# Kernel tuning notes

Measured on AMD Instinct MI355X. Metric: run time of the kernel, lower is better.

The kernel has to match this reference:

```python
import jax, jax.numpy as jnp
import numpy as np

H_IMG, W_IMG = 2160, 3840


def _avgpool3x3(x):
    # AvgPool2d(3, stride=1, padding=1), count_include_pad=True -> divide by 9 always
    s = jax.lax.reduce_window(x, 0.0, jax.lax.add, (3, 3, 1), (1, 1, 1), 'SAME')
    return s / 9.0


def setup_inputs() -> dict:
    key = jax.random.key(0)
    k1, k2, k3, k4 = jax.random.split(key, 4)
    depth = jax.random.uniform(k1, (H_IMG, W_IMG), jnp.float32) * 4.0 + 0.5
    rgb = jax.random.uniform(k2, (H_IMG, W_IMG, 3), jnp.float32)
    mask = jax.random.randint(k3, (H_IMG, W_IMG), 0, 2, jnp.int32)
    l = jax.random.normal(k4, (9, 3), jnp.float32) * 0.3
    fx = fy = 3000.0
    cx, cy = W_IMG / 2.0, H_IMG / 2.0
    CameraParam = jnp.array([[fx, 0.0, cx], [0.0, fy, cy], [0.0, 0.0, 1.0]], jnp.float32)
    return {'depth': depth, 'rgb': rgb, 'mask': mask, 'l': l, 'CameraParam': CameraParam}


def reference(depth, rgb, mask, l, CameraParam):
    nrows, ncols = depth.shape
    imask = mask > 0                      # [H, W] bool
    m3 = imask[..., None]                 # [H, W, 1]

    # Homogeneous pixel grid -> back-projected rays (precomputed in torch __init__)
    yy, xx = jnp.meshgrid(jnp.arange(nrows, dtype=jnp.float32),
                          jnp.arange(ncols, dtype=jnp.float32), indexing='ij')
    p2d = jnp.stack([xx, yy, jnp.ones_like(xx)], axis=-1)      # [H, W, 3]
    Kinv = jnp.linalg.inv(CameraParam)
    p3d = jnp.einsum('ij,hwj->hwi', Kinv, p2d)                 # [H, W, 3]

    # Depth -> 3D points, shifted neighbors (zero-padded at borders)
    p = p3d * depth[..., None]                                 # [H, W, 3]
    pl = jnp.pad(p[:, 1:, :], ((0, 0), (0, 1), (0, 0)))        # right neighbor
    pu = jnp.pad(p[1:, :, :], ((0, 1), (0, 0), (0, 0)))        # down neighbor

    n = jnp.cross(pl - p, pu - p)                              # [H, W, 3]
    norm = jnp.linalg.norm(n, axis=-1, keepdims=True)
    n = n / jnp.maximum(norm, 1e-12)                           # F.normalize

    nx, ny, nz = n[..., 0], n[..., 1], n[..., 2]
    ones = jnp.ones_like(nx)
    Hsh = jnp.stack([ones, ny, nz, nx, nx * ny, ny * nz,
                     -nx * nx - ny * ny + 2.0 * nz * nz,
                     nz * nx, nx * nx - ny * ny], axis=-1)     # [H, W, 9]
    B = jnp.einsum('hwk,kc->hwc', Hsh, l)                      # [H, W, 3]

    # Scatter into full image: zero outside mask (matches render_img[imask] = B)
    render = jnp.where(m3, B, 0.0)
    render_mean = jax.lax.stop_gradient(_avgpool3x3(render))   # render_img.detach()
    rgbmean = _avgpool3x3(jax.lax.stop_gradient(rgb))          # rgb.detach()

    diff = (render - render_mean) - (rgb - rgbmean)
    cnt = jnp.sum(imask).astype(jnp.float32) * 3.0             # MSE over masked elems
    loss = jnp.sum(jnp.where(m3, diff * diff, 0.0)) / cnt
    return loss
```

## Files before the change

### kernel.cpp

```cpp
#include <hip/hip_runtime.h>
#include <math.h>

#define H_IMG 2160
#define W_IMG 3840
#define SPAN 252
#define NSX 16
#define HS 12
#define WPB 4
#define NSY 45
#define NBLOCKS (NSX * NSY)
#define NBINS 2048

__global__ __launch_bounds__(256, 3) void shading_main(
    const float* __restrict__ depth,
    const float* __restrict__ rgb,
    const int*   __restrict__ mask,
    const float* __restrict__ lmat,
    const float* __restrict__ K,
    float* __restrict__ accum,
    int direct)
{
    const int tid  = threadIdx.x;
    const int lane = tid & 63;
    const int wv   = tid >> 6;
    const int sx   = blockIdx.x;
    const int x0   = sx * SPAN;
    const int y0   = blockIdx.y * (WPB * HS) + wv * HS;
    const int colBase = x0 + 4 * lane;
    const bool fullIn = (colBase + 3) < W_IMG;

    const float m00 = K[0], m01 = K[1], m02 = K[2];
    const float m10 = K[3], m11 = K[4], m12 = K[5];
    const float m20 = K[6], m21 = K[7], m22 = K[8];
    const float det = m00*(m11*m22 - m12*m21)
                    - m01*(m10*m22 - m12*m20)
                    + m02*(m10*m21 - m11*m20);
    const float id  = 1.0f / det;
    const float i00 = (m11*m22 - m12*m21) * id;
    const float i01 = (m02*m21 - m01*m22) * id;
    const float i02 = (m01*m12 - m02*m11) * id;
    const float i10 = (m12*m20 - m10*m22) * id;
    const float i11 = (m00*m22 - m02*m20) * id;
    const float i12 = (m02*m10 - m00*m12) * id;
    const float i20 = (m10*m21 - m11*m20) * id;
    const float i21 = (m01*m20 - m00*m21) * id;
    const float i22 = (m00*m11 - m01*m10) * id;

    float L[27];
    #pragma unroll
    for (int i = 0; i < 27; ++i) L[i] = lmat[i];

    float wout[4];
    #pragma unroll
    for (int k = 0; k < 4; ++k) {
        const int c  = colBase + k;
        const int lc = 4 * lane + k;
        const bool v = (c < W_IMG) && (lc <= SPAN) && (lc >= 1 || sx == 0);
        wout[k] = v ? 1.0f : 0.0f;
    }
    const float qm1s = (lane == 0) ? 0.0f : 1.0f;

    float rx = fmaf(i00, (float)colBase, fmaf(i01, (float)(y0 - 1), i02));
    float ry = fmaf(i10, (float)colBase, fmaf(i11, (float)(y0 - 1), i12));
    float rz = fmaf(i20, (float)colBase, fmaf(i21, (float)(y0 - 1), i22));

    const float4 Z4 = make_float4(0.f, 0.f, 0.f, 0.f);

    float4 dC = Z4, dN = Z4;
    float4 raC = Z4, rbC = Z4, rcC = Z4;
    int4   mC  = make_int4(0, 0, 0, 0);
    if (fullIn) {
        if (y0 > 0) {
            const long pix = (long)(y0 - 1) * W_IMG + colBase;
            dC  = *(const float4*)(depth + pix);
            raC = *(const float4*)(rgb + pix * 3);
            rbC = *(const float4*)(rgb + pix * 3 + 4);
            rcC = *(const float4*)(rgb + pix * 3 + 8);
            mC  = *(const int4*)(mask + pix);
        }
        dN = *(const float4*)(depth + (long)y0 * W_IMG + colBase);
    }

    float sA0[4] = {0,0,0,0}, sA1[4] = {0,0,0,0}, sA2[4] = {0,0,0,0};
    float sB0[4] = {0,0,0,0}, sB1[4] = {0,0,0,0}, sB2[4] = {0,0,0,0};
    float qB0[4] = {0,0,0,0}, qB1[4] = {0,0,0,0}, qB2[4] = {0,0,0,0};
    float wB[4]  = {0,0,0,0};
    float accS = 0.f, accC = 0.f;

    #pragma unroll 1
    for (int j = 0; j < HS + 2; ++j) {
        const int h = y0 - 1 + j;

        float4 dP = Z4, raN = Z4, rbN = Z4, rcN = Z4;
        int4   mN = make_int4(0, 0, 0, 0);
        if (fullIn) {
            if (h + 2 < H_IMG)
                dP = *(const float4*)(depth + (long)(h + 2) * W_IMG + colBase);
            if (h + 1 < H_IMG) {
                const long pix = (long)(h + 1) * W_IMG + colBase;
                raN = *(const float4*)(rgb + pix * 3);
                rbN = *(const float4*)(rgb + pix * 3 + 4);
                rcN = *(const float4*)(rgb + pix * 3 + 8);
                mN  = *(const int4*)(mask + pix);
            }
        }

        const float dcv[4] = {dC.x, dC.y, dC.z, dC.w};
        const float dnv[4] = {dN.x, dN.y, dN.z, dN.w};
        const float rrv[12] = {raC.x, raC.y, raC.z, raC.w,
                               rbC.x, rbC.y, rbC.z, rbC.w,
                               rcC.x, rcC.y, rcC.z, rcC.w};
        const int   mmv[4] = {mC.x, mC.y, mC.z, mC.w};
        const float dcR = __shfl_down(dC.x, 1, 64);

        float qC0[4], qC1[4], qC2[4], wC[4];
        float rxk = rx, ryk = ry, rzk = rz;
        #pragma unroll
        for (int k = 0; k < 4; ++k) {
            const float d0 = dcv[k];
            const float dR = (k < 3) ? dcv[k + 1] : dcR;
            const float dD = dnv[k];
            const float px = rxk * d0, py = ryk * d0, pz = rzk * d0;
            const float ax = (rxk + i00) * dR - px;
            const float ay = (ryk + i10) * dR - py;
            const float az = (rzk + i20) * dR - pz;
            const float bx = (rxk + i01) * dD - px;
            const float by = (ryk + i11) * dD - py;
            const float bz = (rzk + i21) * dD - pz;
            float nx = ay*bz - az*by;
            float ny = az*bx - ax*bz;
            float nz = ax*by - ay*bx;
            const float nn  = nx*nx + ny*ny + nz*nz;
            const float inr = __builtin_amdgcn_rsqf(fmaxf(nn, 1e-24f));
            nx *= inr; ny *= inr; nz *= inr;
            const float h4 = nx*ny, h5 = ny*nz, h7 = nz*nx;
            const float nx2 = nx*nx, ny2 = ny*ny, nz2 = nz*nz;
            const float h6 = 2.f*nz2 - nx2 - ny2;
            const float h8 = nx2 - ny2;
            const float B0 = L[0] + ny*L[3] + nz*L[6] + nx*L[9]  + h4*L[12] + h5*L[15] + h6*L[18] + h7*L[21] + h8*L[24];
            const float B1 = L[1] + ny*L[4] + nz*L[7] + nx*L[10] + h4*L[13] + h5*L[16] + h6*L[19] + h7*L[22] + h8*L[25];
            const float B2 = L[2] + ny*L[5] + nz*L[8] + nx*L[11] + h4*L[14] + h5*L[17] + h6*L[20] + h7*L[23] + h8*L[26];
            const float m  = (mmv[k] > 0) ? 1.0f : 0.0f;
            qC0[k] = fmaf(m, B0, -rrv[3*k + 0]);
            qC1[k] = fmaf(m, B1, -rrv[3*k + 1]);
            qC2[k] = fmaf(m, B2, -rrv[3*k + 2]);
            wC[k]  = m * wout[k];
            rxk += i00; ryk += i10; rzk += i20;
        }

        float sC0[4], sC1[4], sC2[4];
        {
            const float a0 = __shfl_up(qC0[3], 1, 64) * qm1s;
            const float a1 = __shfl_up(qC1[3], 1, 64) * qm1s;
            const float a2 = __shfl_up(qC2[3], 1, 64) * qm1s;
            const float p0 = __shfl_down(qC0[0], 1, 64);
            const float p1 = __shfl_down(qC1[0], 1, 64);
            const float p2 = __shfl_down(qC2[0], 1, 64);

            const float t01_0 = qC0[0] + qC0[1];
            const float t12_0 = qC0[1] + qC0[2];
            const float t23_0 = qC0[2] + qC0[3];
            sC0[0] = a0 + t01_0;
            sC0[1] = t01_0 + qC0[2];
            sC0[2] = t12_0 + qC0[3];
            sC0[3] = t23_0 + p0;

            const float t01_1 = qC1[0] + qC1[1];
            const float t12_1 = qC1[1] + qC1[2];
            const float t23_1 = qC1[2] + qC1[3];
            sC1[0] = a1 + t01_1;
            sC1[1] = t01_1 + qC1[2];
            sC1[2] = t12_1 + qC1[3];
            sC1[3] = t23_1 + p1;

            const float t01_2 = qC2[0] + qC2[1];
            const float t12_2 = qC2[1] + qC2[2];
            const float t23_2 = qC2[2] + qC2[3];
            sC2[0] = a2 + t01_2;
            sC2[1] = t01_2 + qC2[2];
            sC2[2] = t12_2 + qC2[3];
            sC2[3] = t23_2 + p2;
        }

        if (j >= 2) {
            #pragma unroll
            for (int k = 0; k < 4; ++k) {
                const float v0 = sA0[k] + sB0[k] + sC0[k];
                const float v1 = sA1[k] + sB1[k] + sC1[k];
                const float v2 = sA2[k] + sB2[k] + sC2[k];
                const float d0 = fmaf(v0, -(1.f/9.f), qB0[k]);
                const float d1 = fmaf(v1, -(1.f/9.f), qB1[k]);
                const float d2 = fmaf(v2, -(1.f/9.f), qB2[k]);
                const float w  = wB[k];
                accS = fmaf(w, d0*d0 + d1*d1 + d2*d2, accS);
                accC += w;
            }
        }

        #pragma unroll
        for (int k = 0; k < 4; ++k) {
            sA0[k] = sB0[k]; sA1[k] = sB1[k]; sA2[k] = sB2[k];
            sB0[k] = sC0[k]; sB1[k] = sC1[k]; sB2[k] = sC2[k];
            qB0[k] = qC0[k]; qB1[k] = qC1[k]; qB2[k] = qC2[k];
            wB[k]  = wC[k];
        }
        dC = dN; dN = dP;
        raC = raN; rbC = rbN; rcC = rcN; mC = mN;
        rx += i01; ry += i11; rz += i21;
    }

    #pragma unroll
    for (int off = 32; off > 0; off >>= 1) {
        accS += __shfl_down(accS, off, 64);
        accC += __shfl_down(accC, off, 64);
    }
    __shared__ float sS[WPB], sC[WPB];
    if (lane == 0) { sS[wv] = accS; sC[wv] = accC; }
    __syncthreads();
    if (tid == 0) {
        const float ts = sS[0] + sS[1] + sS[2] + sS[3];
        const float tc = sC[0] + sC[1] + sC[2] + sC[3];
        const int bid = blockIdx.y * gridDim.x + blockIdx.x;
        if (direct) {
            accum[2*bid + 0] = ts;
            accum[2*bid + 1] = tc;
        } else {
            const int bin = bid & (NBINS - 1);
            atomicAdd(&accum[2*bin + 0], ts);
            atomicAdd(&accum[2*bin + 1], tc);
        }
    }
}

__global__ __launch_bounds__(256) void finalize_kernel(
    const float* __restrict__ part, int n, float* __restrict__ out)
{
    const int tid = threadIdx.x;
    float s = 0.f, c = 0.f;
    for (int i = tid; i < n; i += 256) {
        s += part[2*i + 0];
        c += part[2*i + 1];
    }
    #pragma unroll
    for (int off = 32; off > 0; off >>= 1) {
        s += __shfl_down(s, off, 64);
        c += __shfl_down(c, off, 64);
    }
    __shared__ float sS[4], sC[4];
    const int wid = tid >> 6, lane = tid & 63;
    if (lane == 0) { sS[wid] = s; sC[wid] = c; }
    __syncthreads();
    if (tid == 0) {
        const float ts = sS[0] + sS[1] + sS[2] + sS[3];
        const float tc = sC[0] + sC[1] + sC[2] + sC[3];
        out[0] = ts / (3.0f * tc);
    }
}

extern "C" void kernel_launch(void* const* d_in, const int* in_sizes, int n_in,
                              void* d_out, int out_size, void* d_ws, size_t ws_size,
                              hipStream_t stream) {
    const float* depth = (const float*)d_in[0];
    const float* rgb   = (const float*)d_in[1];
    const int*   mask  = (const int*)  d_in[2];
    const float* lmat  = (const float*)d_in[3];
    const float* K     = (const float*)d_in[4];
    float* accum = (float*)d_ws;
    float* out   = (float*)d_out;

    const dim3 grid(NSX, NSY);

    if (ws_size >= (size_t)NBLOCKS * 2 * sizeof(float)) {
        shading_main<<<grid, 256, 0, stream>>>(depth, rgb, mask, lmat, K, accum, 1);
        finalize_kernel<<<1, 256, 0, stream>>>(accum, NBLOCKS, out);
    } else {
        hipMemsetAsync(accum, 0, NBINS * 2 * sizeof(float), stream);
        shading_main<<<grid, 256, 0, stream>>>(depth, rgb, mask, lmat, K, accum, 0);
        finalize_kernel<<<1, 256, 0, stream>>>(accum, NBINS, out);
    }
}
```

Baseline: 209.0 us.

## Unroll row loop by two with ping-pong registers and relax launch bounds

The row-streaming loop is restructured into pairs of rows, with even and odd register sets that swap roles through a macro body. This removes the per-iteration register rotation of the 3-row window (partial sums, centre values, weights, depth, rgb and mask). Next-row loads are now issued after the normal computation instead of at the top of the loop. Launch bounds drop from 3 to 2 blocks per CU, giving more registers per thread at the cost of occupancy and latency hiding.

Result: no change. 207.3 us (-0.8%).

```diff
diff --git a/kernel.cpp b/kernel.cpp
--- a/kernel.cpp
+++ b/kernel.cpp
@@ -9,9 +9,10 @@
 #define WPB 4
 #define NSY 45
 #define NBLOCKS (NSX * NSY)
+#define NPAIR ((HS + 2) / 2)
 #define NBINS 2048
 
-__global__ __launch_bounds__(256, 3) void shading_main(
+__global__ __launch_bounds__(256, 2) void shading_main(
     const float* __restrict__ depth,
     const float* __restrict__ rgb,
     const int*   __restrict__ mask,
@@ -26,7 +27,8 @@
     const int sx   = blockIdx.x;
     const int x0   = sx * SPAN;
     const int y0   = blockIdx.y * (WPB * HS) + wv * HS;
-    const int colBase = x0 + 4 * lane;
+    const int colBase  = x0 + 4 * lane;
+    const int colBase3 = 3 * colBase;
     const bool fullIn = (colBase + 3) < W_IMG;
 
     const float m00 = K[0], m01 = K[1], m02 = K[2];
@@ -66,148 +68,164 @@
 
     const float4 Z4 = make_float4(0.f, 0.f, 0.f, 0.f);
 
-    float4 dC = Z4, dN = Z4;
-    float4 raC = Z4, rbC = Z4, rcC = Z4;
-    int4   mC  = make_int4(0, 0, 0, 0);
+    float4 dP = Z4, dQ = Z4;
+    float4 raE = Z4, rbE = Z4, rcE = Z4;  int4 mE = make_int4(0,0,0,0);
+    float4 raO = Z4, rbO = Z4, rcO = Z4;  int4 mO = make_int4(0,0,0,0);
+
     if (fullIn) {
-        if (y0 > 0) {
-            const long pix = (long)(y0 - 1) * W_IMG + colBase;
-            dC  = *(const float4*)(depth + pix);
-            raC = *(const float4*)(rgb + pix * 3);
-            rbC = *(const float4*)(rgb + pix * 3 + 4);
-            rcC = *(const float4*)(rgb + pix * 3 + 8);
-            mC  = *(const int4*)(mask + pix);
+        if (y0 > 0 && (y0 - 1) < H_IMG) {
+            const float* dr = depth + (size_t)(y0 - 1) * W_IMG;
+            const float* rr = rgb   + (size_t)(y0 - 1) * (3 * W_IMG);
+            const int*   mr = mask  + (size_t)(y0 - 1) * W_IMG;
+            dP  = *(const float4*)(dr + colBase);
+            raE = *(const float4*)(rr + colBase3);
+            rbE = *(const float4*)(rr + colBase3 + 4);
+            rcE = *(const float4*)(rr + colBase3 + 8);
+            mE  = *(const int4*)(mr + colBase);
         }
-        dN = *(const float4*)(depth + (long)y0 * W_IMG + colBase);
-    }
-
-    float sA0[4] = {0,0,0,0}, sA1[4] = {0,0,0,0}, sA2[4] = {0,0,0,0};
-    float sB0[4] = {0,0,0,0}, sB1[4] = {0,0,0,0}, sB2[4] = {0,0,0,0};
-    float qB0[4] = {0,0,0,0}, qB1[4] = {0,0,0,0}, qB2[4] = {0,0,0,0};
-    float wB[4]  = {0,0,0,0};
+        if (y0 < H_IMG) {
+            const float* dr = depth + (size_t)y0 * W_IMG;
+            const float* rr = rgb   + (size_t)y0 * (3 * W_IMG);
+            const int*   mr = mask  + (size_t)y0 * W_IMG;
+            dQ  = *(const float4*)(dr + colBase);
+            raO = *(const float4*)(rr + colBase3);
+            rbO = *(const float4*)(rr + colBase3 + 4);
+            rcO = *(const float4*)(rr + colBase3 + 8);
+            mO  = *(const int4*)(mr + colBase);
+        }
+    }
+
+    float sE0[4]={0,0,0,0}, sE1[4]={0,0,0,0}, sE2[4]={0,0,0,0};
+    float sO0[4]={0,0,0,0}, sO1[4]={0,0,0,0}, sO2[4]={0,0,0,0};
+    float qE0[4]={0,0,0,0}, qE1[4]={0,0,0,0}, qE2[4]={0,0,0,0};
+    float qO0[4]={0,0,0,0}, qO1[4]={0,0,0,0}, qO2[4]={0,0,0,0};
+    float wE[4]={0,0,0,0},  wO[4]={0,0,0,0};
     float accS = 0.f, accC = 0.f;
 
+#define BODY(DCUR, DNXT, RA, RB, RC, MM, QM0,QM1,QM2, QO0_,QO1_,QO2_, WM, WO_, \
+             SM0,SM1,SM2, SO0_,SO1_,SO2_, ISSROW, DO_EMIT) do {                \
+    const float dcv[4] = {DCUR.x, DCUR.y, DCUR.z, DCUR.w};                     \
+    const float dnv[4] = {DNXT.x, DNXT.y, DNXT.z, DNXT.w};                     \
+    const float rrv[12] = {RA.x,RA.y,RA.z,RA.w, RB.x,RB.y,RB.z,RB.w,           \
+                           RC.x,RC.y,RC.z,RC.w};                               \
+    const int   mmv[4] = {MM.x, MM.y, MM.z, MM.w};                             \
+    const float dcR = __shfl_down(DCUR.x, 1, 64);                              \
+    float rxk = rx, ryk = ry, rzk = rz;                                        \
+    _Pragma("unroll")                                                          \
+    for (int k = 0; k < 4; ++k) {                                              \
+        const float d0 = dcv[k];                                               \
+        const float dR = (k < 3) ? dcv[k + 1] : dcR;                           \
+        const float dD = dnv[k];                                               \
+        const float px = rxk * d0, py = ryk * d0, pz = rzk * d0;               \
+        const float ax = (rxk + i00) * dR - px;                                \
+        const float ay = (ryk + i10) * dR - py;                                \
+        const float az = (rzk + i20) * dR - pz;                                \
+        const float bx = (rxk + i01) * dD - px;                                \
+        const float by = (ryk + i11) * dD - py;                                \
+        const float bz = (rzk + i21) * dD - pz;                                \
+        float nx = ay*bz - az*by;                                              \
+        float ny = az*bx - ax*bz;                                              \
+        float nz = ax*by - ay*bx;                                              \
+        const float nn  = nx*nx + ny*ny + nz*nz;                               \
+        const float inr = __builtin_amdgcn_rsqf(fmaxf(nn, 1e-24f));            \
+        nx *= inr; ny *= inr; nz *= inr;                                       \
+        const float h4 = nx*ny, h5 = ny*nz, h7 = nz*nx;                        \
+        const float nx2 = nx*nx, ny2 = ny*ny, nz2 = nz*nz;                     \
+        const float h6 = 2.f*nz2 - nx2 - ny2;                                  \
+        const float h8 = nx2 - ny2;                                            \
+        const float B0 = L[0] + ny*L[3] + nz*L[6] + nx*L[9]  + h4*L[12]        \
+                       + h5*L[15] + h6*L[18] + h7*L[21] + h8*L[24];            \
+        const float B1 = L[1] + ny*L[4] + nz*L[7] + nx*L[10] + h4*L[13]        \
+                       + h5*L[16] + h6*L[19] + h7*L[22] + h8*L[25];            \
+        const float B2 = L[2] + ny*L[5] + nz*L[8] + nx*L[11] + h4*L[14]        \
+                       + h5*L[17] + h6*L[20] + h7*L[23] + h8*L[26];            \
+        const float m  = (mmv[k] > 0) ? 1.0f : 0.0f;                           \
+        QM0[k] = fmaf(m, B0, -rrv[3*k + 0]);                                   \
+        QM1[k] = fmaf(m, B1, -rrv[3*k + 1]);                                   \
+        QM2[k] = fmaf(m, B2, -rrv[3*k + 2]);                                   \
+        WM[k]  = m * wout[k];                                                  \
+        rxk += i00; ryk += i10; rzk += i20;                                    \
+    }                                                                          \
+             \
+    {                                                                          \
+        const int hI = (ISSROW);                                               \
+        DCUR = Z4; RA = Z4; RB = Z4; RC = Z4; MM = make_int4(0,0,0,0);         \
+        if (fullIn && hI < H_IMG) {                                            \
+            const float* dr = depth + (size_t)hI * W_IMG;                      \
+            const float* rr = rgb   + (size_t)hI * (3 * W_IMG);                \
+            const int*   mr = mask  + (size_t)hI * W_IMG;                      \
+            DCUR = *(const float4*)(dr + colBase);                             \
+            RA   = *(const float4*)(rr + colBase3);                            \
+            RB   = *(const float4*)(rr + colBase3 + 4);                        \
+            RC   = *(const float4*)(rr + colBase3 + 8);                        \
+            MM   = *(const int4*)(mr + colBase);                               \
+        }                                                                      \
+    }                                                                          \
+                                       \
+    float sC0[4], sC1[4], sC2[4];                                              \
+    {                                                                          \
+        const float a0 = __shfl_up(QM0[3], 1, 64) * qm1s;                      \
+        const float a1 = __shfl_up(QM1[3], 1, 64) * qm1s;                      \
+        const float a2 = __shfl_up(QM2[3], 1, 64) * qm1s;                      \
+        const float p0 = __shfl_down(QM0[0], 1, 64);                           \
+        const float p1 = __shfl_down(QM1[0], 1, 64);                           \
+        const float p2 = __shfl_down(QM2[0], 1, 64);                           \
+        const float t01_0 = QM0[0] + QM0[1];                                   \
+        const float t12_0 = QM0[1] + QM0[2];                                   \
+        const float t23_0 = QM0[2] + QM0[3];                                   \
+        sC0[0] = a0 + t01_0;                                                   \
+        sC0[1] = t01_0 + QM0[2];                                               \
+        sC0[2] = t12_0 + QM0[3];                                               \
+        sC0[3] = t23_0 + p0;                                                   \
+        const float t01_1 = QM1[0] + QM1[1];                                   \
+        const float t12_1 = QM1[1] + QM1[2];                                   \
+        const float t23_1 = QM1[2] + QM1[3];                                   \
+        sC1[0] = a1 + t01_1;                                                   \
+        sC1[1] = t01_1 + QM1[2];                                               \
+        sC1[2] = t12_1 + QM1[3];                                               \
+        sC1[3] = t23_1 + p1;                                                   \
+        const float t01_2 = QM2[0] + QM2[1];                                   \
+        const float t12_2 = QM2[1] + QM2[2];                                   \
+        const float t23_2 = QM2[2] + QM2[3];                                   \
+        sC2[0] = a2 + t01_2;                                                   \
+        sC2[1] = t01_2 + QM2[2];                                               \
+        sC2[2] = t12_2 + QM2[3];                                               \
+        sC2[3] = t23_2 + p2;                                                   \
+    }                                                                          \
+           \
+    if (DO_EMIT) {                                                             \
+        _Pragma("unroll")                                                      \
+        for (int k = 0; k < 4; ++k) {                                          \
+            const float v0 = SM0[k] + SO0_[k] + sC0[k];                        \
+            const float v1 = SM1[k] + SO1_[k] + sC1[k];                        \
+            const float v2 = SM2[k] + SO2_[k] + sC2[k];                        \
+            const float d0 = fmaf(v0, -(1.f/9.f), QO0_[k]);                    \
+            const float d1 = fmaf(v1, -(1.f/9.f), QO1_[k]);                    \
+            const float d2 = fmaf(v2, -(1.f/9.f), QO2_[k]);                    \
+            const float w  = WO_[k];                                           \
+            accS = fmaf(w, d0*d0 + d1*d1 + d2*d2, accS);                       \
+            accC += w;                                                         \
+        }                                                                      \
+    }                                                                          \
+    _Pragma("unroll")                                                          \
+    for (int k = 0; k < 4; ++k) { SM0[k] = sC0[k]; SM1[k] = sC1[k];            \
+                                  SM2[k] = sC2[k]; }                           \
+    rx += i01; ry += i11; rz += i21;                                           \
+} while (0)
+
+    int hP = y0 + 1;
     #pragma unroll 1
-    for (int j = 0; j < HS + 2; ++j) {
-        const int h = y0 - 1 + j;
-
-        float4 dP = Z4, raN = Z4, rbN = Z4, rcN = Z4;
-        int4   mN = make_int4(0, 0, 0, 0);
-        if (fullIn) {
-            if (h + 2 < H_IMG)
-                dP = *(const float4*)(depth + (long)(h + 2) * W_IMG + colBase);
-            if (h + 1 < H_IMG) {
-                const long pix = (long)(h + 1) * W_IMG + colBase;
-                raN = *(const float4*)(rgb + pix * 3);
-                rbN = *(const float4*)(rgb + pix * 3 + 4);
-                rcN = *(const float4*)(rgb + pix * 3 + 8);
-                mN  = *(const int4*)(mask + pix);
-            }
-        }
-
-        const float dcv[4] = {dC.x, dC.y, dC.z, dC.w};
-        const float dnv[4] = {dN.x, dN.y, dN.z, dN.w};
-        const float rrv[12] = {raC.x, raC.y, raC.z, raC.w,
-                               rbC.x, rbC.y, rbC.z, rbC.w,
-                               rcC.x, rcC.y, rcC.z, rcC.w};
-        const int   mmv[4] = {mC.x, mC.y, mC.z, mC.w};
-        const float dcR = __shfl_down(dC.x, 1, 64);
-
-        float qC0[4], qC1[4], qC2[4], wC[4];
-        float rxk = rx, ryk = ry, rzk = rz;
-        #pragma unroll
-        for (int k = 0; k < 4; ++k) {
-            const float d0 = dcv[k];
-            const float dR = (k < 3) ? dcv[k + 1] : dcR;
-            const float dD = dnv[k];
-            const float px = rxk * d0, py = ryk * d0, pz = rzk * d0;
-            const float ax = (rxk + i00) * dR - px;
-            const float ay = (ryk + i10) * dR - py;
-            const float az = (rzk + i20) * dR - pz;
-            const float bx = (rxk + i01) * dD - px;
-            const float by = (ryk + i11) * dD - py;
-            const float bz = (rzk + i21) * dD - pz;
-            float nx = ay*bz - az*by;
-            float ny = az*bx - ax*bz;
-            float nz = ax*by - ay*bx;
-            const float nn  = nx*nx + ny*ny + nz*nz;
-            const float inr = __builtin_amdgcn_rsqf(fmaxf(nn, 1e-24f));
-            nx *= inr; ny *= inr; nz *= inr;
-            const float h4 = nx*ny, h5 = ny*nz, h7 = nz*nx;
-            const float nx2 = nx*nx, ny2 = ny*ny, nz2 = nz*nz;
-            const float h6 = 2.f*nz2 - nx2 - ny2;
-            const float h8 = nx2 - ny2;
-            const float B0 = L[0] + ny*L[3] + nz*L[6] + nx*L[9]  + h4*L[12] + h5*L[15] + h6*L[18] + h7*L[21] + h8*L[24];
-            const float B1 = L[1] + ny*L[4] + nz*L[7] + nx*L[10] + h4*L[13] + h5*L[16] + h6*L[19] + h7*L[22] + h8*L[25];
-            const float B2 = L[2] + ny*L[5] + nz*L[8] + nx*L[11] + h4*L[14] + h5*L[17] + h6*L[20] + h7*L[23] + h8*L[26];
-            const float m  = (mmv[k] > 0) ? 1.0f : 0.0f;
-            qC0[k] = fmaf(m, B0, -rrv[3*k + 0]);
-            qC1[k] = fmaf(m, B1, -rrv[3*k + 1]);
-            qC2[k] = fmaf(m, B2, -rrv[3*k + 2]);
-            wC[k]  = m * wout[k];
-            rxk += i00; ryk += i10; rzk += i20;
-        }
-
-        float sC0[4], sC1[4], sC2[4];
-        {
-            const float a0 = __shfl_up(qC0[3], 1, 64) * qm1s;
-            const float a1 = __shfl_up(qC1[3], 1, 64) * qm1s;
-            const float a2 = __shfl_up(qC2[3], 1, 64) * qm1s;
-            const float p0 = __shfl_down(qC0[0], 1, 64);
-            const float p1 = __shfl_down(qC1[0], 1, 64);
-            const float p2 = __shfl_down(qC2[0], 1, 64);
-
-            const float t01_0 = qC0[0] + qC0[1];
-            const float t12_0 = qC0[1] + qC0[2];
-            const float t23_0 = qC0[2] + qC0[3];
-            sC0[0] = a0 + t01_0;
-            sC0[1] = t01_0 + qC0[2];
-            sC0[2] = t12_0 + qC0[3];
-            sC0[3] = t23_0 + p0;
-
-            const float t01_1 = qC1[0] + qC1[1];
-            const float t12_1 = qC1[1] + qC1[2];
-            const float t23_1 = qC1[2] + qC1[3];
-            sC1[0] = a1 + t01_1;
-            sC1[1] = t01_1 + qC1[2];
-            sC1[2] = t12_1 + qC1[3];
-            sC1[3] = t23_1 + p1;
-
-            const float t01_2 = qC2[0] + qC2[1];
-            const float t12_2 = qC2[1] + qC2[2];
-            const float t23_2 = qC2[2] + qC2[3];
-            sC2[0] = a2 + t01_2;
-            sC2[1] = t01_2 + qC2[2];
-            sC2[2] = t12_2 + qC2[3];
-            sC2[3] = t23_2 + p2;
-        }
-
-        if (j >= 2) {
-            #pragma unroll
-            for (int k = 0; k < 4; ++k) {
-                const float v0 = sA0[k] + sB0[k] + sC0[k];
-                const float v1 = sA1[k] + sB1[k] + sC1[k];
-                const float v2 = sA2[k] + sB2[k] + sC2[k];
-                const float d0 = fmaf(v0, -(1.f/9.f), qB0[k]);
-                const float d1 = fmaf(v1, -(1.f/9.f), qB1[k]);
-                const float d2 = fmaf(v2, -(1.f/9.f), qB2[k]);
-                const float w  = wB[k];
-                accS = fmaf(w, d0*d0 + d1*d1 + d2*d2, accS);
-                accC += w;
-            }
-        }
-
-        #pragma unroll
-        for (int k = 0; k < 4; ++k) {
-            sA0[k] = sB0[k]; sA1[k] = sB1[k]; sA2[k] = sB2[k];
-            sB0[k] = sC0[k]; sB1[k] = sC1[k]; sB2[k] = sC2[k];
-            qB0[k] = qC0[k]; qB1[k] = qC1[k]; qB2[k] = qC2[k];
-            wB[k]  = wC[k];
-        }
-        dC = dN; dN = dP;
-        raC = raN; rbC = rbN; rcC = rcN; mC = mN;
-        rx += i01; ry += i11; rz += i21;
-    }
+    for (int t = 0; t < NPAIR; ++t) {
+        const bool em = (t >= 1);
+        BODY(dP, dQ, raE, rbE, rcE, mE,
+             qE0, qE1, qE2, qO0, qO1, qO2, wE, wO,
+             sE0, sE1, sE2, sO0, sO1, sO2, hP, em);
+        BODY(dQ, dP, raO, rbO, rcO, mO,
+             qO0, qO1, qO2, qE0, qE1, qE2, wO, wE,
+             sO0, sO1, sO2, sE0, sE1, sE2, hP + 1, em);
+        hP += 2;
+    }
+#undef BODY
 
     #pragma unroll
     for (int off = 32; off > 0; off >>= 1) {
```
